# Kernel tuning notes

Hardware: AMD Instinct MI355X
Metric: run time of the kernel (lower is better)

Reference implementation:

```python
import jax, jax.numpy as jnp
import numpy as np

N, K, H, T = 65536, 8, 128, 4  # nodes, max children, h_size, n_types


def setup_inputs() -> dict:
    key = jax.random.key(0)
    ks = jax.random.split(key, 8)
    h = jax.random.normal(ks[0], (N, K, H), jnp.float32)          # mailbox child hidden states
    c = jax.random.normal(ks[1], (N, K, H), jnp.float32)          # mailbox child cell states
    f_input = jax.random.normal(ks[2], (N, H), jnp.float32)       # precomputed x @ W_f per node
    type_id = jax.random.randint(ks[3], (N,), 0, T, jnp.int32)    # node type for dispatch
    scale = 0.05
    U_iou = jax.random.normal(ks[4], (T, H, 3 * H), jnp.float32) * scale  # per-type i,o,u recurrent mats
    b_iou = jax.random.normal(ks[5], (T, 3 * H), jnp.float32) * scale
    U_f = jax.random.normal(ks[6], (T, H, H), jnp.float32) * scale        # per-type forget-gate mat
    b_f = jax.random.normal(ks[7], (T, H), jnp.float32) * scale
    return dict(h=h, c=c, f_input=f_input, type_id=type_id,
                U_iou=U_iou, b_iou=b_iou, U_f=U_f, b_f=b_f)


def reference(h, c, f_input, type_id, U_iou, b_iou, U_f, b_f):
    """TypedTreeCell.reduce_func: per-type TreeLSTM child aggregation.

    Returns concat([iou_aggr, c_aggr], -1) of shape [N, 4*H].
    """
    n_types = U_iou.shape[0]
    n_nodes = h.shape[0]
    h_size = h.shape[2]
    h_sum = h.sum(axis=1)  # [N, H] child-sum for i,o,u gates
    iou_aggr = jnp.zeros((n_nodes, 3 * h_size), h.dtype)
    c_aggr = jnp.zeros((n_nodes, h_size), h.dtype)
    for t in range(n_types):  # fixed small type loop mirrors the module's dispatch
        m = (type_id == t)[:, None]
        iou_t = h_sum @ U_iou[t] + b_iou[t]                                  # [N, 3H]
        f_t = jax.nn.sigmoid(f_input[:, None, :] + h @ U_f[t] + b_f[t])     # [N, K, H]
        c_t = (f_t * c).sum(axis=1)                                          # [N, H]
        iou_aggr = jnp.where(m, iou_t, iou_aggr)
        c_aggr = jnp.where(m, c_t, c_aggr)
    return jnp.concatenate([iou_aggr, c_aggr], axis=-1)
```

## Files before the change

### kernel.cpp

```cpp
#include <hip/hip_runtime.h>
#include <cstdint>


typedef __bf16 bf16;
typedef bf16 bf16x8 __attribute__((ext_vector_type(8)));
typedef bf16 bf16x4 __attribute__((ext_vector_type(4)));
typedef float f32x4 __attribute__((ext_vector_type(4)));

#define N_NODES 65536
#define KCH 8
#define HSZ 128
#define T_TYPES 4
#define TM 16
#define LDS_STRIDE 136

#define WS_PERM_OFF   256
#define WS_PREUF_OFF  (WS_PERM_OFF + 4*N_NODES)
#define WS_PREUIOU_OFF (WS_PREUF_OFF + 131072)

__global__ void k_count(const int* __restrict__ ta, int* __restrict__ ws_i) {
    int i = blockIdx.x * blockDim.x + threadIdx.x;
    int t = ta[i];
    int lane = threadIdx.x & 63;
    #pragma unroll
    for (int tt = 0; tt < T_TYPES; ++tt) {
        unsigned long long m = __ballot(t == tt);
        int leader = __ffsll((unsigned long long)m) - 1;
        if (t == tt && lane == leader)
            atomicAdd(&ws_i[tt], (int)__popcll(m));
    }
}

__global__ void k_offsets(int* ws_i) {
    if (threadIdx.x == 0 && blockIdx.x == 0) {
        int acc = 0, tacc = 0;
        for (int t = 0; t < T_TYPES; ++t) {
            int cnt = ws_i[t];
            ws_i[8 + t] = acc;
            ws_i[4 + t] = acc;
            ws_i[12 + t] = tacc;
            acc += cnt;
            tacc += (cnt + TM - 1) / TM;
        }
        ws_i[16] = tacc;
    }
}

__global__ void k_scatter(const int* __restrict__ ta, int* __restrict__ ws_i,
                          int* __restrict__ perm) {
    int i = blockIdx.x * blockDim.x + threadIdx.x;
    int t = ta[i];
    int lane = threadIdx.x & 63;
    #pragma unroll
    for (int tt = 0; tt < T_TYPES; ++tt) {
        unsigned long long m = __ballot(t == tt);
        if (t == tt) {
            int leader = __ffsll((unsigned long long)m) - 1;
            int base = 0;
            if (lane == leader) base = atomicAdd(&ws_i[4 + tt], (int)__popcll(m));
            base = __shfl(base, leader, 64);
            int rank = (int)__popcll(m & ((1ull << lane) - 1ull));
            perm[base + rank] = i;
        }
    }
}

__global__ void k_swz(const float* __restrict__ Uf, const float* __restrict__ Uiou,
                      bf16* __restrict__ dstf, bf16* __restrict__ dstiou) {
    int idx = blockIdx.x * blockDim.x + threadIdx.x;
    if (idx < T_TYPES * HSZ * HSZ) {
        int t = idx >> 14;
        int r = (idx >> 7) & 127;
        int j = idx & 127;
        float v = Uf[idx];
        int kblk = r >> 5, kin = r & 31;
        int lane = ((kin >> 3) << 4) | (j & 15);
        int e = kin & 7;
        int cb = j >> 4;
        dstf[((((t * 4 + kblk) * 8 + cb) * 64 + lane) << 3) + e] = (bf16)v;
    } else {
        int i2 = idx - T_TYPES * HSZ * HSZ;
        int t = i2 / 49152;
        int rm = i2 - t * 49152;
        int r = rm / 384;
        int j = rm - r * 384;
        float v = Uiou[i2];
        int kblk = r >> 5, kin = r & 31;
        int lane = ((kin >> 3) << 4) | (j & 15);
        int e = kin & 7;
        int cb = j >> 4;
        dstiou[((((t * 4 + kblk) * 24 + cb) * 64 + lane) << 3) + e] = (bf16)v;
    }
}

__global__ __launch_bounds__(512, 4) void k_main(
    const float* __restrict__ h, const float* __restrict__ c,
    const float* __restrict__ f_input,
    const float* __restrict__ b_iou, const float* __restrict__ b_f,
    const int* __restrict__ perm, const int* __restrict__ ws_i,
    const bf16* __restrict__ preUf, const bf16* __restrict__ preUiou,
    float* __restrict__ out)
{
    const int b = blockIdx.x;
    if (b >= ws_i[16]) return;
    int t;
    if (b < ws_i[13]) t = 0;
    else if (b < ws_i[14]) t = 1;
    else if (b < ws_i[15]) t = 2;
    else t = 3;
    const int tile = b - ws_i[12 + t];
    const int cnt = ws_i[t];
    const int base = ws_i[8 + t] + tile * TM;
    const int rem = min(TM, cnt - tile * TM);

    __shared__ __align__(16) bf16 hs[(128 + 16) * LDS_STRIDE];
    bf16* hsum = hs + 128 * LDS_STRIDE;

    const int tid = threadIdx.x;
    const int w2 = tid >> 6;
    const int l = tid & 63;
    const int lu = l & 15;
    const int g = l >> 4;

    {
        int node = w2 * 2 + (g >> 1);
        int khalf = (g & 1) * 4;
        int mc = node < rem ? node : 0;
        long gn = perm[base + mc];
        const float* hp = h + gn * (long)(KCH * HSZ) + lu * 8;
        float sarr[8];
        #pragma unroll
        for (int i = 0; i < 8; ++i) sarr[i] = 0.f;
        #pragma unroll
        for (int k0 = 0; k0 < 4; ++k0) {
            int k = khalf + k0;
            const float4* p = (const float4*)(hp + k * HSZ);
            float4 a = p[0], bb = p[1];
            sarr[0] += a.x; sarr[1] += a.y; sarr[2] += a.z; sarr[3] += a.w;
            sarr[4] += bb.x; sarr[5] += bb.y; sarr[6] += bb.z; sarr[7] += bb.w;
            bf16x8 v;
            v[0] = (bf16)a.x; v[1] = (bf16)a.y; v[2] = (bf16)a.z; v[3] = (bf16)a.w;
            v[4] = (bf16)bb.x; v[5] = (bf16)bb.y; v[6] = (bf16)bb.z; v[7] = (bf16)bb.w;
            *((bf16x8*)&hs[(node * KCH + k) * LDS_STRIDE + lu * 8]) = v;
        }
        #pragma unroll
        for (int i = 0; i < 8; ++i) sarr[i] += __shfl_xor(sarr[i], 16, 64);
        if ((g & 1) == 0) {
            bf16x8 sv;
            #pragma unroll
            for (int i = 0; i < 8; ++i) sv[i] = (bf16)sarr[i];
            *((bf16x8*)&hsum[node * LDS_STRIDE + lu * 8]) = sv;
        }
    }
    __syncthreads();

    f32x4 acc[4][2];
    #pragma unroll
    for (int rt = 0; rt < 4; ++rt)
        #pragma unroll
        for (int cb = 0; cb < 2; ++cb)
            acc[rt][cb] = (f32x4){0.f, 0.f, 0.f, 0.f};

    const int rbase = (w2 >> 2) * 4;
    const int cpair = (w2 & 3);
    const bf16x8* Bf = (const bf16x8*)preUf;
    #pragma unroll
    for (int kb = 0; kb < 4; ++kb) {
        bf16x8 b0 = Bf[((t * 4 + kb) * 8 + cpair * 2 + 0) * 64 + l];
        bf16x8 b1 = Bf[((t * 4 + kb) * 8 + cpair * 2 + 1) * 64 + l];
        #pragma unroll
        for (int rt = 0; rt < 4; ++rt) {
            bf16x8 a = *((const bf16x8*)&hs[((rbase + rt) * 16 + lu) * LDS_STRIDE + kb * 32 + g * 8]);
            acc[rt][0] = __builtin_amdgcn_mfma_f32_16x16x32_bf16(a, b0, acc[rt][0], 0, 0, 0);
            acc[rt][1] = __builtin_amdgcn_mfma_f32_16x16x32_bf16(a, b1, acc[rt][1], 0, 0, 0);
        }
    }

    f32x4 acc2[3];
    #pragma unroll
    for (int cf = 0; cf < 3; ++cf) acc2[cf] = (f32x4){0.f, 0.f, 0.f, 0.f};
    const bf16x8* Bi = (const bf16x8*)preUiou;
    #pragma unroll
    for (int kb = 0; kb < 4; ++kb) {
        bf16x8 a = *((const bf16x8*)&hsum[lu * LDS_STRIDE + kb * 32 + g * 8]);
        #pragma unroll
        for (int cf = 0; cf < 3; ++cf) {
            bf16x8 bfr = Bi[((t * 4 + kb) * 24 + w2 * 3 + cf) * 64 + l];
            acc2[cf] = __builtin_amdgcn_mfma_f32_16x16x32_bf16(a, bfr, acc2[cf], 0, 0, 0);
        }
    }
    {
        long gns[4]; bool ok[4];
        #pragma unroll
        for (int r = 0; r < 4; ++r) {
            int m = g * 4 + r;
            ok[r] = m < rem;
            gns[r] = perm[base + (ok[r] ? m : 0)];
        }
        #pragma unroll
        for (int cf = 0; cf < 3; ++cf) {
            int col = (w2 * 3 + cf) * 16 + lu;
            float bi = b_iou[t * 384 + col];
            #pragma unroll
            for (int r = 0; r < 4; ++r)
                if (ok[r]) out[gns[r] * (4 * HSZ) + col] = acc2[cf][r] + bi;
        }
    }

    __syncthreads();
    {
        const int col0 = cpair * 32 + lu;
        const float bf0 = b_f[t * HSZ + col0];
        const float bf1 = b_f[t * HSZ + col0 + 16];
        #pragma unroll
        for (int rt = 0; rt < 4; ++rt) {
            #pragma unroll
            for (int cb = 0; cb < 2; ++cb) {
                #pragma unroll
                for (int r = 0; r < 4; ++r) {
                    int rc = (rbase + rt) * 16 + g * 4 + r;
                    float s = acc[rt][cb][r] + (cb ? bf1 : bf0);
                    hs[rc * LDS_STRIDE + col0 + cb * 16] = (bf16)s;
                }
            }
        }
    }
    __syncthreads();

    {
        int m = tid >> 5;
        int cg = tid & 31;
        bool ok = m < rem;
        long gn = perm[base + (ok ? m : 0)];
        const float* crow = c + gn * (long)(KCH * HSZ) + cg * 4;
        float4 fi = *(const float4*)(f_input + gn * HSZ + cg * 4);
        float4 accv = {0.f, 0.f, 0.f, 0.f};
        #pragma unroll
        for (int k = 0; k < KCH; ++k) {
            bf16x4 sv = *(const bf16x4*)&hs[(m * KCH + k) * LDS_STRIDE + cg * 4];
            float4 cv = *(const float4*)(crow + k * HSZ);
            float s0 = (float)sv[0] + fi.x;
            float s1 = (float)sv[1] + fi.y;
            float s2 = (float)sv[2] + fi.z;
            float s3 = (float)sv[3] + fi.w;
            accv.x += cv.x / (1.f + __expf(-s0));
            accv.y += cv.y / (1.f + __expf(-s1));
            accv.z += cv.z / (1.f + __expf(-s2));
            accv.w += cv.w / (1.f + __expf(-s3));
        }
        if (ok) *((float4*)(out + gn * (4 * HSZ) + 3 * HSZ + cg * 4)) = accv;
    }
}

extern "C" void kernel_launch(void* const* d_in, const int* in_sizes, int n_in,
                              void* d_out, int out_size, void* d_ws, size_t ws_size,
                              hipStream_t stream) {
    const float* h       = (const float*)d_in[0];
    const float* c       = (const float*)d_in[1];
    const float* f_input = (const float*)d_in[2];
    const int*   type_id = (const int*)d_in[3];
    const float* U_iou   = (const float*)d_in[4];
    const float* b_iou   = (const float*)d_in[5];
    const float* U_f     = (const float*)d_in[6];
    const float* b_f     = (const float*)d_in[7];
    float* out = (float*)d_out;

    char* ws = (char*)d_ws;
    int* ws_i = (int*)ws;
    int* perm = (int*)(ws + WS_PERM_OFF);
    bf16* preUf = (bf16*)(ws + WS_PREUF_OFF);
    bf16* preUiou = (bf16*)(ws + WS_PREUIOU_OFF);

    hipMemsetAsync(ws, 0, 128, stream);
    k_swz    <<<(T_TYPES * HSZ * HSZ + T_TYPES * HSZ * 3 * HSZ) / 256, 256, 0, stream>>>(U_f, U_iou, preUf, preUiou);
    k_count  <<<N_NODES / 256, 256, 0, stream>>>(type_id, ws_i);
    k_offsets<<<1, 64, 0, stream>>>(ws_i);
    k_scatter<<<N_NODES / 256, 256, 0, stream>>>(type_id, ws_i, perm);

    k_main<<<N_NODES / TM + T_TYPES, 512, 0, stream>>>(h, c, f_input, b_iou, b_f,
                                                       perm, ws_i, preUf, preUiou, out);
}
```

Before: 712.4 us.

## Fuse forget-gate epilogue into MFMA registers, drop LDS round-trip and syncs

The forget-gate sigmoid and the weighted sum over c are now computed straight from the MFMA accumulator registers. This replaces writing bf16 pre-activations to LDS, two barriers, and re-reading them. Each lane loads its own c and f_input elements and reduces the two child halves with a cross-lane shuffle. Node indices are cached in LDS instead of being re-read from perm, the bias is kept in fp32, division becomes a hardware reciprocal, and the launch bound asks for 6 blocks per SM. The risk is that c loads become scalar and strided rather than float4-coalesced, and the tighter launch bound may force register spills.

```diff
diff --git a/kernel.cpp b/kernel.cpp
--- a/kernel.cpp
+++ b/kernel.cpp
@@ -93,7 +93,7 @@
     }
 }
 
-__global__ __launch_bounds__(512, 4) void k_main(
+__global__ __launch_bounds__(512, 6) void k_main(
     const float* __restrict__ h, const float* __restrict__ c,
     const float* __restrict__ f_input,
     const float* __restrict__ b_iou, const float* __restrict__ b_f,
@@ -114,6 +114,7 @@
     const int rem = min(TM, cnt - tile * TM);
 
     __shared__ __align__(16) bf16 hs[(128 + 16) * LDS_STRIDE];
+    __shared__ int gn_lds[TM];
     bf16* hsum = hs + 128 * LDS_STRIDE;
 
     const int tid = threadIdx.x;
@@ -126,8 +127,9 @@
         int node = w2 * 2 + (g >> 1);
         int khalf = (g & 1) * 4;
         int mc = node < rem ? node : 0;
-        long gn = perm[base + mc];
-        const float* hp = h + gn * (long)(KCH * HSZ) + lu * 8;
+        int gn = perm[base + mc];
+        if (lu == 0 && (g & 1) == 0) gn_lds[node] = gn;
+        const float* hp = h + (long)gn * (KCH * HSZ) + lu * 8;
         float sarr[8];
         #pragma unroll
         for (int i = 0; i < 8; ++i) sarr[i] = 0.f;
@@ -189,66 +191,64 @@
             acc2[cf] = __builtin_amdgcn_mfma_f32_16x16x32_bf16(a, bfr, acc2[cf], 0, 0, 0);
         }
     }
+
     {
-        long gns[4]; bool ok[4];
-        #pragma unroll
-        for (int r = 0; r < 4; ++r) {
-            int m = g * 4 + r;
-            ok[r] = m < rem;
-            gns[r] = perm[base + (ok[r] ? m : 0)];
-        }
         #pragma unroll
         for (int cf = 0; cf < 3; ++cf) {
             int col = (w2 * 3 + cf) * 16 + lu;
             float bi = b_iou[t * 384 + col];
             #pragma unroll
-            for (int r = 0; r < 4; ++r)
-                if (ok[r]) out[gns[r] * (4 * HSZ) + col] = acc2[cf][r] + bi;
-        }
-    }
-
-    __syncthreads();
+            for (int r = 0; r < 4; ++r) {
+                int m = g * 4 + r;
+                if (m < rem)
+                    out[(long)gn_lds[m] * (4 * HSZ) + col] = acc2[cf][r] + bi;
+            }
+        }
+    }
+
     {
         const int col0 = cpair * 32 + lu;
-        const float bf0 = b_f[t * HSZ + col0];
-        const float bf1 = b_f[t * HSZ + col0 + 16];
+        const float bfv0 = b_f[t * HSZ + col0];
+        const float bfv1 = b_f[t * HSZ + col0 + 16];
+        const int ghalf = g >> 1;
+        const int kbase = (g & 1) * 4;
+
+        int nd[4]; bool ok2[4]; long gns2[4];
         #pragma unroll
         for (int rt = 0; rt < 4; ++rt) {
-            #pragma unroll
-            for (int cb = 0; cb < 2; ++cb) {
-                #pragma unroll
-                for (int r = 0; r < 4; ++r) {
-                    int rc = (rbase + rt) * 16 + g * 4 + r;
-                    float s = acc[rt][cb][r] + (cb ? bf1 : bf0);
-                    hs[rc * LDS_STRIDE + col0 + cb * 16] = (bf16)s;
-                }
-            }
-        }
-    }
-    __syncthreads();
-
-    {
-        int m = tid >> 5;
-        int cg = tid & 31;
-        bool ok = m < rem;
-        long gn = perm[base + (ok ? m : 0)];
-        const float* crow = c + gn * (long)(KCH * HSZ) + cg * 4;
-        float4 fi = *(const float4*)(f_input + gn * HSZ + cg * 4);
-        float4 accv = {0.f, 0.f, 0.f, 0.f};
-        #pragma unroll
-        for (int k = 0; k < KCH; ++k) {
-            bf16x4 sv = *(const bf16x4*)&hs[(m * KCH + k) * LDS_STRIDE + cg * 4];
-            float4 cv = *(const float4*)(crow + k * HSZ);
-            float s0 = (float)sv[0] + fi.x;
-            float s1 = (float)sv[1] + fi.y;
-            float s2 = (float)sv[2] + fi.z;
-            float s3 = (float)sv[3] + fi.w;
-            accv.x += cv.x / (1.f + __expf(-s0));
-            accv.y += cv.y / (1.f + __expf(-s1));
-            accv.z += cv.z / (1.f + __expf(-s2));
-            accv.w += cv.w / (1.f + __expf(-s3));
-        }
-        if (ok) *((float4*)(out + gn * (4 * HSZ) + 3 * HSZ + cg * 4)) = accv;
+            nd[rt] = (rbase + rt) * 2 + ghalf;
+            ok2[rt] = nd[rt] < rem;
+            gns2[rt] = gn_lds[nd[rt]];
+        }
+
+        #pragma unroll
+        for (int rt = 0; rt < 4; ++rt) {
+            const float* fr = f_input + gns2[rt] * HSZ + col0;
+            float fi0 = fr[0];
+            float fi1 = fr[16];
+            const float* crow = c + gns2[rt] * (long)(KCH * HSZ) + kbase * HSZ + col0;
+            float cv0[4], cv1[4];
+            #pragma unroll
+            for (int r = 0; r < 4; ++r) {
+                cv0[r] = crow[r * HSZ];
+                cv1[r] = crow[r * HSZ + 16];
+            }
+            float p0 = 0.f, p1 = 0.f;
+            #pragma unroll
+            for (int r = 0; r < 4; ++r) {
+                float s0 = acc[rt][0][r] + fi0 + bfv0;
+                float s1 = acc[rt][1][r] + fi1 + bfv1;
+                p0 += cv0[r] * __builtin_amdgcn_rcpf(1.f + __expf(-s0));
+                p1 += cv1[r] * __builtin_amdgcn_rcpf(1.f + __expf(-s1));
+            }
+            p0 += __shfl_xor(p0, 16, 64);
+            p1 += __shfl_xor(p1, 16, 64);
+            if ((g & 1) == 0 && ok2[rt]) {
+                float* orow = out + gns2[rt] * (4 * HSZ) + 3 * HSZ + col0;
+                orow[0] = p0;
+                orow[16] = p1;
+            }
+        }
     }
 }
 
```

Measured after the change: 713.5 us. No clear change (+0.1%).
